# Kernel tuning notes

Hardware: AMD Instinct MI355X
Metric: run time of the kernel (lower is better)

Reference implementation:

```python
import jax, jax.numpy as jnp
import numpy as np

N, E, D, H, Z = 20000, 320000, 512, 512, 128
SCALING_FACTOR = 1.0


def setup_inputs() -> dict:
    key = jax.random.key(0)
    ks = jax.random.split(key, 12)
    def glorot(k, fi, fo):
        lim = float(np.sqrt(6.0 / (fi + fo)))
        return jax.random.uniform(k, (fi, fo), jnp.float32, -lim, lim)
    return {
        "x": jax.random.normal(ks[0], (N, D), jnp.float32),
        "edge_index": jax.random.randint(ks[1], (2, E), 0, N, jnp.int32),
        "eps": jax.random.normal(ks[2], (N, Z), jnp.float32),
        "W1": glorot(ks[3], D, H), "b1": jnp.zeros((H,), jnp.float32),
        "W2": glorot(ks[4], H, H), "b2": jnp.zeros((H,), jnp.float32),
        "Wmu": glorot(ks[5], H, Z), "bmu": jnp.zeros((Z,), jnp.float32),
        "Wlv": glorot(ks[6], H, Z), "blv": jnp.zeros((Z,), jnp.float32),
    }


def reference(x, edge_index, eps, W1, b1, W2, b2, Wmu, bmu, Wlv, blv):
    n = x.shape[0]
    src, dst = edge_index[0], edge_index[1]
    # GCN symmetric normalization with added self-loops (PyG GCNConv default)
    deg = jax.ops.segment_sum(jnp.ones(src.shape[0], x.dtype), dst, num_segments=n) + 1.0
    dinv = jax.lax.rsqrt(deg)                      # deg^{-1/2}, deg >= 1
    edge_coef = dinv[src] * dinv[dst]              # [E]
    self_coef = dinv * dinv                        # [N] self-loop weight

    def gcn(h, W, b):
        h = h @ W                                  # linear first, then propagate
        agg = jax.ops.segment_sum(h[src] * edge_coef[:, None], dst, num_segments=n)
        return agg + self_coef[:, None] * h + b

    # hidden layer 0: relu -> dropout(eval=identity) -> L2 normalize * scaling
    h = jax.nn.relu(gcn(x, W1, b1))
    h = h / jnp.maximum(jnp.linalg.norm(h, axis=1, keepdims=True), 1e-12) * SCALING_FACTOR
    # hidden layer 1 (last): relu only
    h = jax.nn.relu(gcn(h, W2, b2))
    # GaussianSample: GCN heads for mu / log_var, reparameterized sample
    mu = gcn(h, Wmu, bmu)
    log_var = gcn(h, Wlv, blv)
    z = mu + eps * jnp.exp(0.5 * log_var)
    return z, mu, log_var
```

## Files before the change

kernel.cpp:

```cpp
#include <hip/hip_runtime.h>

typedef __bf16 bf16x8 __attribute__((ext_vector_type(8)));
typedef __bf16 bf16x4 __attribute__((ext_vector_type(4)));
typedef float  f32x4  __attribute__((ext_vector_type(4)));
typedef float  f32x2  __attribute__((ext_vector_type(2)));

#define GLDS16(g, l) __builtin_amdgcn_global_load_lds( \
    (const __attribute__((address_space(1))) void*)(g), \
    (__attribute__((address_space(3))) void*)(l), 16, 0, 0)

#define FP8_SCALE 64.0f
#define FP8_INV   (1.0f / 64.0f)

__device__ __forceinline__ unsigned char fp8_of_f32(float v) {
  return (unsigned char)(__builtin_amdgcn_cvt_pk_fp8_f32(v, v, 0, false) & 0xff);
}
__device__ __forceinline__ void dec4(unsigned int u, float* o) {
  f32x2 lo = __builtin_amdgcn_cvt_pk_f32_fp8(u, false);
  f32x2 hi = __builtin_amdgcn_cvt_pk_f32_fp8(u, true);
  o[0] = lo[0]; o[1] = lo[1]; o[2] = hi[0]; o[3] = hi[1];
}


__global__ void count_kernel(const int* __restrict__ dst, int* __restrict__ cnt, int E) {
  int idx = blockIdx.x * blockDim.x + threadIdx.x;
  int stride = gridDim.x * blockDim.x;
  for (int e = idx; e < E; e += stride) atomicAdd(&cnt[dst[e]], 1);
}

__global__ __launch_bounds__(1024) void scan1_kernel(const int* __restrict__ cnt,
                                                     int* __restrict__ rowptr,
                                                     float* __restrict__ dinv,
                                                     int* __restrict__ bsum, int n) {
  __shared__ int wsum[16];
  const int t = threadIdx.x, b = blockIdx.x;
  const int gid = b * 1024 + t;
  const int lane = t & 63, w = t >> 6;
  int val = (gid < n) ? cnt[gid] : 0;
  if (gid < n) dinv[gid] = rsqrtf((float)val + 1.0f);
  int incl = val;
  #pragma unroll
  for (int off = 1; off < 64; off <<= 1) {
    int u = __shfl_up(incl, off);
    if (lane >= off) incl += u;
  }
  if (lane == 63) wsum[w] = incl;
  __syncthreads();
  if (w == 0) {
    int v = (lane < 16) ? wsum[lane] : 0;
    int iv = v;
    #pragma unroll
    for (int off = 1; off < 16; off <<= 1) {
      int u = __shfl_up(iv, off);
      if (lane >= off) iv += u;
    }
    if (lane < 16) wsum[lane] = iv - v;
    if (lane == 15) bsum[b] = iv;
  }
  __syncthreads();
  if (gid < n) rowptr[gid] = wsum[w] + incl - val;
}

__global__ void scan2_kernel(const int* __restrict__ bsum, int* __restrict__ boff,
                             int* __restrict__ rowptr, int nb, int n) {
  if (threadIdx.x == 0 && blockIdx.x == 0) {
    int run = 0;
    for (int b = 0; b < nb; b++) { boff[b] = run; run += bsum[b]; }
    rowptr[n] = run;
  }
}

__global__ __launch_bounds__(1024) void scan3_kernel(int* __restrict__ rowptr,
                                                     const int* __restrict__ boff, int n) {
  int gid = blockIdx.x * 1024 + threadIdx.x;
  if (gid < n) rowptr[gid] += boff[blockIdx.x];
}

__global__ void fill_kernel(const int* __restrict__ src, const int* __restrict__ dst,
                            const int* __restrict__ rowptr, int* __restrict__ cur,
                            const float* __restrict__ dinv,
                            int2* __restrict__ csr_pack, int E) {
  int idx = blockIdx.x * blockDim.x + threadIdx.x;
  int stride = gridDim.x * blockDim.x;
  for (int e = idx; e < E; e += stride) {
    int s = src[e], d = dst[e];
    int slot = rowptr[d] + atomicAdd(&cur[d], 1);
    int2 p; p.x = s; p.y = __float_as_int(dinv[s] * dinv[d] * FP8_INV);
    csr_pack[slot] = p;
  }
}


__global__ void convert_kernel(const float* __restrict__ x,
                               const float* __restrict__ W1, const float* __restrict__ W2,
                               const float* __restrict__ Wmu, const float* __restrict__ Wlv,
                               __bf16* __restrict__ xb,
                               __bf16* __restrict__ w1t, __bf16* __restrict__ w2t,
                               __bf16* __restrict__ wct) {
  int id = blockIdx.x * blockDim.x + threadIdx.x;
  if (id < 2621440) {
    float4 v = ((const float4*)x)[id];
    bf16x4 b;
    b[0] = (__bf16)v.x; b[1] = (__bf16)v.y; b[2] = (__bf16)v.z; b[3] = (__bf16)v.w;
    ((bf16x4*)xb)[id] = b;
  } else {
    int t = id - 2621440;
    if (t < 262144) {
      int nn = t >> 9, kk = t & 511;
      w1t[t] = (__bf16)W1[kk * 512 + nn];
    } else if (t < 524288) {
      int u = t - 262144;
      int nn = u >> 9, kk = u & 511;
      w2t[u] = (__bf16)W2[kk * 512 + nn];
    } else {
      int u = t - 524288;
      int nn = u >> 9, kk = u & 511;
      float v = (nn < 128) ? Wmu[kk * 128 + nn] : Wlv[kk * 128 + (nn - 128)];
      wct[u] = (__bf16)v;
    }
  }
}


__global__ __launch_bounds__(256, 4) void gemm_bt(const __bf16* __restrict__ A,
                                                  const __bf16* __restrict__ Bt,
                                                  unsigned char* __restrict__ C,
                                                  int M, int N, int K, int ntiles_n) {
  __shared__ __align__(16) __bf16 sA[2][128 * 32];
  __shared__ __align__(16) __bf16 sB[2][128 * 32];
  const int nb = gridDim.x;
  const int orig = blockIdx.x;
  const int q = nb >> 3, r = nb & 7;
  const int xcd = orig & 7, sub = orig >> 3;
  const int pos = (xcd < r) ? (xcd * (q + 1) + sub) : (r * (q + 1) + (xcd - r) * q + sub);
  const int m0 = (pos / ntiles_n) * 128, n0 = (pos % ntiles_n) * 128;

  const int tid = threadIdx.x;
  const int wave = tid >> 6, lane = tid & 63;
  const int wr = wave >> 1, wc = wave & 1;
  f32x4 acc[4][4] = {};
  const int srow = lane >> 2;
  const int sg   = (lane & 3) ^ ((srow >> 1) & 3);
  const int nt = K >> 5;

  auto STAGE = [&](int b, int k0) {
    #pragma unroll
    for (int c = 0; c < 2; ++c) {
      int chunk = wave * 2 + c;
      int row = chunk * 16 + srow;
      int ga = m0 + row; if (ga >= M) ga = M - 1;
      GLDS16(A  + (long)ga * K         + k0 + sg * 8, sA[b] + chunk * 512);
      GLDS16(Bt + (long)(n0 + row) * K + k0 + sg * 8, sB[b] + chunk * 512);
    }
  };

  STAGE(0, 0);
  for (int t = 0; t < nt; ++t) {
    const int cur = t & 1;
    if (t + 1 < nt) {
      STAGE(cur ^ 1, (t + 1) << 5);
      asm volatile("s_waitcnt vmcnt(4)" ::: "memory");
    } else {
      asm volatile("s_waitcnt vmcnt(0)" ::: "memory");
    }
    __builtin_amdgcn_s_barrier();
    __builtin_amdgcn_sched_barrier(0);

    const int fr = lane & 15, gbase = lane >> 4;
    const int gs = gbase ^ ((fr >> 1) & 3);
    bf16x8 af[4], bfr[4];
    #pragma unroll
    for (int mi = 0; mi < 4; mi++)
      af[mi] = *(const bf16x8*)(sA[cur] + (wr * 64 + mi * 16 + fr) * 32 + gs * 8);
    #pragma unroll
    for (int ni = 0; ni < 4; ni++)
      bfr[ni] = *(const bf16x8*)(sB[cur] + (wc * 64 + ni * 16 + fr) * 32 + gs * 8);
    #pragma unroll
    for (int mi = 0; mi < 4; mi++)
      #pragma unroll
      for (int ni = 0; ni < 4; ni++)
        acc[mi][ni] = __builtin_amdgcn_mfma_f32_16x16x32_bf16(af[mi], bfr[ni], acc[mi][ni], 0, 0, 0);
    asm volatile("s_waitcnt lgkmcnt(0)" ::: "memory");
    __builtin_amdgcn_sched_barrier(0);
    __builtin_amdgcn_s_barrier();
  }

  const int crow0 = (lane >> 4) * 4, ccol = lane & 15;
  #pragma unroll
  for (int mi = 0; mi < 4; mi++)
    #pragma unroll
    for (int ni = 0; ni < 4; ni++)
      #pragma unroll
      for (int r2 = 0; r2 < 4; r2++) {
        int row = m0 + wr * 64 + mi * 16 + crow0 + r2;
        if (row < M)
          C[(long)row * N + n0 + wc * 64 + ni * 16 + ccol] =
              fp8_of_f32(acc[mi][ni][r2] * FP8_SCALE);
      }
}


template<int EPL> struct LSel;
template<> struct LSel<8> { typedef uint2 T; };
template<> struct LSel<4> { typedef unsigned int T; };

template<int EPL, int MODE>
__global__ __launch_bounds__(512) void prop_kernel(
    const unsigned char* __restrict__ Cin, const int* __restrict__ rowptr,
    const int2* __restrict__ csr_pack,
    const float* __restrict__ dinv, const float* __restrict__ bias,
    const float* __restrict__ bmu, const float* __restrict__ blv,
    const float* __restrict__ eps,
    __bf16* __restrict__ hout, float* __restrict__ zout, int n) {
  constexpr int F = EPL * 64;
  typedef typename LSel<EPL>::T VecT;
  const int lane = threadIdx.x & 63;
  const int i = blockIdx.x * (blockDim.x >> 6) + (threadIdx.x >> 6);
  if (i >= n) return;
  const unsigned char* __restrict__ Clane = Cin + lane * EPL;

  auto decAll = [&](VecT v, float* o) {
    if constexpr (EPL == 8) { dec4(v.x, o); dec4(v.y, o + 4); }
    else                    { dec4(v, o); }
  };

  float acc[EPL];
  {
    const float di = dinv[i];
    const float sc = di * di * FP8_INV;
    VecT v = *(const VecT*)(Clane + (size_t)i * F);
    float dv[EPL];
    decAll(v, dv);
    #pragma unroll
    for (int j = 0; j < EPL; j++) acc[j] = sc * dv[j];
  }
  int e = rowptr[i];
  const int e1 = rowptr[i + 1];
  for (; e + 8 <= e1; e += 8) {
    int2 p[8];
    #pragma unroll
    for (int q = 0; q < 8; q++) p[q] = csr_pack[e + q];
    VecT v[8];
    #pragma unroll
    for (int q = 0; q < 8; q++) v[q] = *(const VecT*)(Clane + (size_t)p[q].x * F);
    #pragma unroll
    for (int q = 0; q < 8; q++) {
      float c = __int_as_float(p[q].y);
      float dv[EPL];
      decAll(v[q], dv);
      #pragma unroll
      for (int j = 0; j < EPL; j++) acc[j] += c * dv[j];
    }
  }
  for (; e + 4 <= e1; e += 4) {
    int2 p[4];
    #pragma unroll
    for (int q = 0; q < 4; q++) p[q] = csr_pack[e + q];
    VecT v[4];
    #pragma unroll
    for (int q = 0; q < 4; q++) v[q] = *(const VecT*)(Clane + (size_t)p[q].x * F);
    #pragma unroll
    for (int q = 0; q < 4; q++) {
      float c = __int_as_float(p[q].y);
      float dv[EPL];
      decAll(v[q], dv);
      #pragma unroll
      for (int j = 0; j < EPL; j++) acc[j] += c * dv[j];
    }
  }
  for (; e < e1; ++e) {
    int2 p = csr_pack[e];
    float c = __int_as_float(p.y);
    VecT v = *(const VecT*)(Clane + (size_t)p.x * F);
    float dv[EPL];
    decAll(v, dv);
    #pragma unroll
    for (int j = 0; j < EPL; j++) acc[j] += c * dv[j];
  }

  if constexpr (MODE == 0 || MODE == 1) {
    float ss = 0.f;
    #pragma unroll
    for (int j = 0; j < EPL; j++) {
      acc[j] += bias[lane * EPL + j];
      acc[j] = fmaxf(acc[j], 0.f);
      ss += acc[j] * acc[j];
    }
    float scale = 1.f;
    if constexpr (MODE == 0) {
      #pragma unroll
      for (int off = 32; off > 0; off >>= 1) ss += __shfl_xor(ss, off);
      scale = 1.f / fmaxf(sqrtf(ss), 1e-12f);
    }
    bf16x8 o;
    #pragma unroll
    for (int j = 0; j < EPL; j++) o[j] = (__bf16)(acc[j] * scale);
    *(bf16x8*)(hout + (size_t)i * 512 + lane * EPL) = o;
  } else {
    const bool ismu = lane < 32;
    const int cb4 = (ismu ? lane : lane - 32) * 4;
    float v[4];
    #pragma unroll
    for (int j = 0; j < 4; j++) v[j] = acc[j] + (ismu ? bmu[cb4 + j] : blv[cb4 + j]);
    const size_t NZ = (size_t)n * 128;
    float* dstp = ismu ? (zout + NZ + (size_t)i * 128 + cb4)
                       : (zout + 2 * NZ + (size_t)i * 128 + cb4);
    float4 st; st.x = v[0]; st.y = v[1]; st.z = v[2]; st.w = v[3];
    *(float4*)dstp = st;
    float ov[4];
    #pragma unroll
    for (int j = 0; j < 4; j++) ov[j] = __shfl_xor(v[j], 32);
    if (ismu) {
      float4 ev = *(const float4*)(eps + (size_t)i * 128 + cb4);
      float4 zs;
      zs.x = v[0] + ev.x * expf(0.5f * ov[0]);
      zs.y = v[1] + ev.y * expf(0.5f * ov[1]);
      zs.z = v[2] + ev.z * expf(0.5f * ov[2]);
      zs.w = v[3] + ev.w * expf(0.5f * ov[3]);
      *(float4*)(zout + (size_t)i * 128 + cb4) = zs;
    }
  }
}


extern "C" void kernel_launch(void* const* d_in, const int* in_sizes, int n_in,
                              void* d_out, int out_size, void* d_ws, size_t ws_size,
                              hipStream_t stream) {
  const float* x   = (const float*)d_in[0];
  const int*   ei  = (const int*)d_in[1];
  const float* eps = (const float*)d_in[2];
  const float* W1  = (const float*)d_in[3];
  const float* b1  = (const float*)d_in[4];
  const float* W2  = (const float*)d_in[5];
  const float* b2  = (const float*)d_in[6];
  const float* Wmu = (const float*)d_in[7];
  const float* bmu = (const float*)d_in[8];
  const float* Wlv = (const float*)d_in[9];
  const float* blv = (const float*)d_in[10];
  float* out = (float*)d_out;

  const int N = 20000, E = 320000, D = 512, H = 512, Z = 128;
  const int* src = ei;
  const int* dst = ei + E;
  const int NB = (N + 1023) / 1024;

  char* p = (char*)d_ws;
  auto alloc = [&](size_t bytes) { char* r = p; p += (bytes + 255) & ~(size_t)255; return r; };
  int*    cnt      = (int*)alloc((size_t)N * 4);
  int*    cur      = (int*)alloc((size_t)N * 4);
  int*    rowptr   = (int*)alloc((size_t)(N + 1) * 4);
  float*  dinv     = (float*)alloc((size_t)N * 4);
  int*    bsum     = (int*)alloc((size_t)NB * 4);
  int*    boff     = (int*)alloc((size_t)NB * 4);
  int2*   csr_pack = (int2*)alloc((size_t)E * 8);
  __bf16* xb  = (__bf16*)alloc((size_t)N * D * 2);
  __bf16* hb  = (__bf16*)alloc((size_t)N * H * 2);
  unsigned char* cb = (unsigned char*)alloc((size_t)N * H);
  __bf16* w1t = (__bf16*)alloc((size_t)D * H * 2);
  __bf16* w2t = (__bf16*)alloc((size_t)H * H * 2);
  __bf16* wct = (__bf16*)alloc((size_t)2 * Z * H * 2);

  hipMemsetAsync(cnt, 0, (size_t)N * 4, stream);
  hipMemsetAsync(cur, 0, (size_t)N * 4, stream);

  count_kernel<<<1250, 256, 0, stream>>>(dst, cnt, E);
  scan1_kernel<<<NB, 1024, 0, stream>>>(cnt, rowptr, dinv, bsum, N);
  scan2_kernel<<<1, 64, 0, stream>>>(bsum, boff, rowptr, NB, N);
  scan3_kernel<<<NB, 1024, 0, stream>>>(rowptr, boff, N);
  fill_kernel<<<1250, 256, 0, stream>>>(src, dst, rowptr, cur, dinv, csr_pack, E);
  convert_kernel<<<12800, 256, 0, stream>>>(x, W1, W2, Wmu, Wlv, xb, w1t, w2t, wct);

  gemm_bt<<<((N + 127) / 128) * (H / 128), 256, 0, stream>>>(xb, w1t, cb, N, H, D, H / 128);
  prop_kernel<8, 0><<<2500, 512, 0, stream>>>(cb, rowptr, csr_pack, dinv,
                                              b1, nullptr, nullptr, nullptr, hb, nullptr, N);
  gemm_bt<<<((N + 127) / 128) * (H / 128), 256, 0, stream>>>(hb, w2t, cb, N, H, H, H / 128);
  prop_kernel<8, 1><<<2500, 512, 0, stream>>>(cb, rowptr, csr_pack, dinv,
                                              b2, nullptr, nullptr, nullptr, xb, nullptr, N);
  gemm_bt<<<((N + 127) / 128) * ((2 * Z) / 128), 256, 0, stream>>>(xb, wct, cb, N, 2 * Z, H, (2 * Z) / 128);
  prop_kernel<4, 2><<<2500, 512, 0, stream>>>(cb, rowptr, csr_pack, dinv,
                                              nullptr, bmu, blv, eps, nullptr, out, N);
}
```

Baseline: 202.0 us.

## Fuse preprocessing kernels and overlap CSR fill with first GEMM

Merges edge counting, weight transpose/convert (now via an LDS-tiled transpose) and x conversion into one prep kernel. It also merges the scan fixup steps into a single kernel, and co-launches the CSR fill as extra blocks of the first GEMM kernel. Both memsets become one because cnt and cur sit next to each other in the workspace. The aim is fewer launches and letting the irregular fill run alongside the GEMM, at the cost of those blocks competing with the GEMM and a serial per-block prefix loop.

```diff
diff --git a/kernel.cpp b/kernel.cpp
--- a/kernel.cpp
+++ b/kernel.cpp
@@ -22,11 +22,46 @@
 }
 
 
-__global__ void count_kernel(const int* __restrict__ dst, int* __restrict__ cnt, int E) {
-  int idx = blockIdx.x * blockDim.x + threadIdx.x;
-  int stride = gridDim.x * blockDim.x;
-  for (int e = idx; e < E; e += stride) atomicAdd(&cnt[dst[e]], 1);
-}
+#define CNT_BLKS 640
+#define WT_BLKS  640
+
+__global__ __launch_bounds__(256) void prep_kernel(
+    const int* __restrict__ dstv, int* __restrict__ cnt, int E,
+    const float* __restrict__ x, __bf16* __restrict__ xb,
+    const float* __restrict__ W1, const float* __restrict__ W2,
+    const float* __restrict__ Wmu, const float* __restrict__ Wlv,
+    __bf16* __restrict__ w1t, __bf16* __restrict__ w2t, __bf16* __restrict__ wct) {
+  const int b = blockIdx.x;
+  if (b < CNT_BLKS) {
+    int idx = b * 256 + threadIdx.x;
+    for (int e = idx; e < E; e += CNT_BLKS * 256) atomicAdd(&cnt[dstv[e]], 1);
+  } else if (b < CNT_BLKS + WT_BLKS) {
+    __shared__ float tile[32][33];
+    int t = b - CNT_BLKS;
+    const float* S; __bf16* D; int kt, ntl, drow, snw;
+    if (t < 256)      { S = W1;  D = w1t; kt = t & 15;        ntl = t >> 4;        drow = ntl * 32;       snw = 512; }
+    else if (t < 512) { int u = t - 256; S = W2;  D = w2t; kt = u & 15; ntl = u >> 4; drow = ntl * 32;       snw = 512; }
+    else if (t < 576) { int u = t - 512; S = Wmu; D = wct; kt = u & 15; ntl = u >> 4; drow = ntl * 32;       snw = 128; }
+    else              { int u = t - 576; S = Wlv; D = wct; kt = u & 15; ntl = u >> 4; drow = 128 + ntl * 32; snw = 128; }
+    const int k0 = kt * 32, n0 = ntl * 32;
+    const int r = threadIdx.x >> 5, c = threadIdx.x & 31;
+    #pragma unroll
+    for (int p = 0; p < 4; p++)
+      tile[r + p * 8][c] = S[(k0 + r + p * 8) * snw + n0 + c];
+    __syncthreads();
+    #pragma unroll
+    for (int p = 0; p < 4; p++)
+      D[(drow + r + p * 8) * 512 + k0 + c] = (__bf16)tile[c][r + p * 8];
+  } else {
+    int id = (b - CNT_BLKS - WT_BLKS) * 256 + threadIdx.x;
+    if (id < 2560000) {
+      float4 v = ((const float4*)x)[id];
+      bf16x4 o; o[0] = (__bf16)v.x; o[1] = (__bf16)v.y; o[2] = (__bf16)v.z; o[3] = (__bf16)v.w;
+      ((bf16x4*)xb)[id] = o;
+    }
+  }
+}
+
 
 __global__ __launch_bounds__(1024) void scan1_kernel(const int* __restrict__ cnt,
                                                      int* __restrict__ rowptr,
@@ -61,75 +96,30 @@
   if (gid < n) rowptr[gid] = wsum[w] + incl - val;
 }
 
-__global__ void scan2_kernel(const int* __restrict__ bsum, int* __restrict__ boff,
-                             int* __restrict__ rowptr, int nb, int n) {
-  if (threadIdx.x == 0 && blockIdx.x == 0) {
+__global__ __launch_bounds__(1024) void scan23_kernel(int* __restrict__ rowptr,
+                                                      const int* __restrict__ bsum,
+                                                      int n, int nb) {
+  __shared__ int off_s;
+  const int b = blockIdx.x;
+  if (threadIdx.x == 0) {
     int run = 0;
-    for (int b = 0; b < nb; b++) { boff[b] = run; run += bsum[b]; }
-    rowptr[n] = run;
-  }
-}
-
-__global__ __launch_bounds__(1024) void scan3_kernel(int* __restrict__ rowptr,
-                                                     const int* __restrict__ boff, int n) {
-  int gid = blockIdx.x * 1024 + threadIdx.x;
-  if (gid < n) rowptr[gid] += boff[blockIdx.x];
-}
-
-__global__ void fill_kernel(const int* __restrict__ src, const int* __restrict__ dst,
-                            const int* __restrict__ rowptr, int* __restrict__ cur,
-                            const float* __restrict__ dinv,
-                            int2* __restrict__ csr_pack, int E) {
-  int idx = blockIdx.x * blockDim.x + threadIdx.x;
-  int stride = gridDim.x * blockDim.x;
-  for (int e = idx; e < E; e += stride) {
-    int s = src[e], d = dst[e];
-    int slot = rowptr[d] + atomicAdd(&cur[d], 1);
-    int2 p; p.x = s; p.y = __float_as_int(dinv[s] * dinv[d] * FP8_INV);
-    csr_pack[slot] = p;
-  }
-}
-
-
-__global__ void convert_kernel(const float* __restrict__ x,
-                               const float* __restrict__ W1, const float* __restrict__ W2,
-                               const float* __restrict__ Wmu, const float* __restrict__ Wlv,
-                               __bf16* __restrict__ xb,
-                               __bf16* __restrict__ w1t, __bf16* __restrict__ w2t,
-                               __bf16* __restrict__ wct) {
-  int id = blockIdx.x * blockDim.x + threadIdx.x;
-  if (id < 2621440) {
-    float4 v = ((const float4*)x)[id];
-    bf16x4 b;
-    b[0] = (__bf16)v.x; b[1] = (__bf16)v.y; b[2] = (__bf16)v.z; b[3] = (__bf16)v.w;
-    ((bf16x4*)xb)[id] = b;
-  } else {
-    int t = id - 2621440;
-    if (t < 262144) {
-      int nn = t >> 9, kk = t & 511;
-      w1t[t] = (__bf16)W1[kk * 512 + nn];
-    } else if (t < 524288) {
-      int u = t - 262144;
-      int nn = u >> 9, kk = u & 511;
-      w2t[u] = (__bf16)W2[kk * 512 + nn];
-    } else {
-      int u = t - 524288;
-      int nn = u >> 9, kk = u & 511;
-      float v = (nn < 128) ? Wmu[kk * 128 + nn] : Wlv[kk * 128 + (nn - 128)];
-      wct[u] = (__bf16)v;
-    }
-  }
-}
-
-
-__global__ __launch_bounds__(256, 4) void gemm_bt(const __bf16* __restrict__ A,
-                                                  const __bf16* __restrict__ Bt,
-                                                  unsigned char* __restrict__ C,
-                                                  int M, int N, int K, int ntiles_n) {
+    for (int i = 0; i < b; i++) run += bsum[i];
+    off_s = run;
+    if (b == nb - 1) rowptr[n] = run + bsum[b];
+  }
+  __syncthreads();
+  int gid = b * 1024 + threadIdx.x;
+  if (gid < n) rowptr[gid] += off_s;
+}
+
+
+__device__ __forceinline__ void gemm_tile(int orig, int nb,
+                                          const __bf16* __restrict__ A,
+                                          const __bf16* __restrict__ Bt,
+                                          unsigned char* __restrict__ C,
+                                          int M, int N, int K, int ntiles_n) {
   __shared__ __align__(16) __bf16 sA[2][128 * 32];
   __shared__ __align__(16) __bf16 sB[2][128 * 32];
-  const int nb = gridDim.x;
-  const int orig = blockIdx.x;
   const int q = nb >> 3, r = nb & 7;
   const int xcd = orig & 7, sub = orig >> 3;
   const int pos = (xcd < r) ? (xcd * (q + 1) + sub) : (r * (q + 1) + (xcd - r) * q + sub);
@@ -143,14 +133,14 @@
   const int sg   = (lane & 3) ^ ((srow >> 1) & 3);
   const int nt = K >> 5;
 
-  auto STAGE = [&](int b, int k0) {
+  auto STAGE = [&](int bb, int k0) {
     #pragma unroll
     for (int c = 0; c < 2; ++c) {
       int chunk = wave * 2 + c;
       int row = chunk * 16 + srow;
       int ga = m0 + row; if (ga >= M) ga = M - 1;
-      GLDS16(A  + (long)ga * K         + k0 + sg * 8, sA[b] + chunk * 512);
-      GLDS16(Bt + (long)(n0 + row) * K + k0 + sg * 8, sB[b] + chunk * 512);
+      GLDS16(A  + (long)ga * K         + k0 + sg * 8, sA[bb] + chunk * 512);
+      GLDS16(Bt + (long)(n0 + row) * K + k0 + sg * 8, sB[bb] + chunk * 512);
     }
   };
 
@@ -197,6 +187,33 @@
           C[(long)row * N + n0 + wc * 64 + ni * 16 + ccol] =
               fp8_of_f32(acc[mi][ni][r2] * FP8_SCALE);
       }
+}
+
+__global__ __launch_bounds__(256, 4) void gemm_bt(const __bf16* __restrict__ A,
+                                                  const __bf16* __restrict__ Bt,
+                                                  unsigned char* __restrict__ C,
+                                                  int M, int N, int K, int ntiles_n, int ngb) {
+  gemm_tile(blockIdx.x, ngb, A, Bt, C, M, N, K, ntiles_n);
+}
+
+__global__ __launch_bounds__(256, 4) void gemm1_fill_kernel(
+    const __bf16* __restrict__ A, const __bf16* __restrict__ Bt,
+    unsigned char* __restrict__ C, int M, int N, int K, int ntiles_n, int ngb,
+    const int* __restrict__ src, const int* __restrict__ dstv,
+    const int* __restrict__ rowptr, int* __restrict__ cur,
+    const float* __restrict__ dinv, int2* __restrict__ csr_pack, int E) {
+  if (blockIdx.x < (unsigned)ngb) {
+    gemm_tile(blockIdx.x, ngb, A, Bt, C, M, N, K, ntiles_n);
+  } else {
+    int idx = (blockIdx.x - ngb) * 256 + threadIdx.x;
+    int stride = (gridDim.x - ngb) * 256;
+    for (int e = idx; e < E; e += stride) {
+      int s = src[e], d = dstv[e];
+      int slot = rowptr[d] + atomicAdd(&cur[d], 1);
+      int2 p; p.x = s; p.y = __float_as_int(dinv[s] * dinv[d] * FP8_INV);
+      csr_pack[slot] = p;
+    }
+  }
 }
 
 
@@ -351,7 +368,6 @@
   int*    rowptr   = (int*)alloc((size_t)(N + 1) * 4);
   float*  dinv     = (float*)alloc((size_t)N * 4);
   int*    bsum     = (int*)alloc((size_t)NB * 4);
-  int*    boff     = (int*)alloc((size_t)NB * 4);
   int2*   csr_pack = (int2*)alloc((size_t)E * 8);
   __bf16* xb  = (__bf16*)alloc((size_t)N * D * 2);
   __bf16* hb  = (__bf16*)alloc((size_t)N * H * 2);
@@ -360,23 +376,24 @@
   __bf16* w2t = (__bf16*)alloc((size_t)H * H * 2);
   __bf16* wct = (__bf16*)alloc((size_t)2 * Z * H * 2);
 
-  hipMemsetAsync(cnt, 0, (size_t)N * 4, stream);
-  hipMemsetAsync(cur, 0, (size_t)N * 4, stream);
-
-  count_kernel<<<1250, 256, 0, stream>>>(dst, cnt, E);
+  hipMemsetAsync(cnt, 0, ((size_t)N * 4 + 255 & ~(size_t)255) + (size_t)N * 4, stream);
+
+  prep_kernel<<<CNT_BLKS + WT_BLKS + 10000, 256, 0, stream>>>(
+      dst, cnt, E, x, xb, W1, W2, Wmu, Wlv, w1t, w2t, wct);
   scan1_kernel<<<NB, 1024, 0, stream>>>(cnt, rowptr, dinv, bsum, N);
-  scan2_kernel<<<1, 64, 0, stream>>>(bsum, boff, rowptr, NB, N);
-  scan3_kernel<<<NB, 1024, 0, stream>>>(rowptr, boff, N);
-  fill_kernel<<<1250, 256, 0, stream>>>(src, dst, rowptr, cur, dinv, csr_pack, E);
-  convert_kernel<<<12800, 256, 0, stream>>>(x, W1, W2, Wmu, Wlv, xb, w1t, w2t, wct);
-
-  gemm_bt<<<((N + 127) / 128) * (H / 128), 256, 0, stream>>>(xb, w1t, cb, N, H, D, H / 128);
+  scan23_kernel<<<NB, 1024, 0, stream>>>(rowptr, bsum, N, NB);
+
+  const int NGB1 = ((N + 127) / 128) * (H / 128);
+  gemm1_fill_kernel<<<NGB1 + 1250, 256, 0, stream>>>(
+      xb, w1t, cb, N, H, D, H / 128, NGB1,
+      src, dst, rowptr, cur, dinv, csr_pack, E);
   prop_kernel<8, 0><<<2500, 512, 0, stream>>>(cb, rowptr, csr_pack, dinv,
                                               b1, nullptr, nullptr, nullptr, hb, nullptr, N);
-  gemm_bt<<<((N + 127) / 128) * (H / 128), 256, 0, stream>>>(hb, w2t, cb, N, H, H, H / 128);
+  gemm_bt<<<NGB1, 256, 0, stream>>>(hb, w2t, cb, N, H, H, H / 128, NGB1);
   prop_kernel<8, 1><<<2500, 512, 0, stream>>>(cb, rowptr, csr_pack, dinv,
                                               b2, nullptr, nullptr, nullptr, xb, nullptr, N);
-  gemm_bt<<<((N + 127) / 128) * ((2 * Z) / 128), 256, 0, stream>>>(xb, wct, cb, N, 2 * Z, H, (2 * Z) / 128);
+  const int NGB3 = ((N + 127) / 128) * ((2 * Z) / 128);
+  gemm_bt<<<NGB3, 256, 0, stream>>>(xb, wct, cb, N, 2 * Z, H, (2 * Z) / 128, NGB3);
   prop_kernel<4, 2><<<2500, 512, 0, stream>>>(cb, rowptr, csr_pack, dinv,
                                               nullptr, bmu, blv, eps, nullptr, out, N);
 }
```

Result: faster. 182.2 us (-9.8%).
